# Kernel tuning notes

Hardware: AMD Instinct MI355X
Metric: run time of the kernel (lower is better)

## Reference

```python
import jax, jax.numpy as jnp
import numpy as np

DIM = 512
HEADS = 8
HEAD = DIM // HEADS
T = 243          # temporal length, fixed by get_temporal_mask(243, ...)
N_JOINTS = 17    # skeleton joints
BATCH = 4        # number of clips; leading dim of x is BATCH*T
WINDOWS = (9, 27, 81, 243)  # temporal_MoE_type


def _temporal_masks():
    # Block-diagonal window masks: 0 inside each window block, -100000 outside,
    # exactly matching get_temporal_mask + torch.where(matrix == 0, -100000, 0).
    idx = np.arange(T)
    masks = np.stack([
        np.where((idx[:, None] // w) == (idx[None, :] // w), 0.0, -100000.0)
        for w in WINDOWS
    ]).astype(np.float32)  # (E, T, T)
    return jnp.asarray(masks)


def setup_inputs() -> dict:
    key = jax.random.key(0)
    k0, k1, k2, k3 = jax.random.split(key, 4)
    scaled = lambda k, shape, fan: jax.random.normal(k, shape, jnp.float32) * (fan ** -0.5)
    return {
        "x": jax.random.normal(k0, (BATCH * T, N_JOINTS, DIM), jnp.float32),
        "qkv_w": scaled(k1, (DIM, 3 * DIM), DIM),          # qkv (no bias, qkv_bias=False)
        "proj_w": scaled(k2, (DIM, DIM), DIM),             # output projection
        "proj_b": jnp.zeros((DIM,), jnp.float32),
        "te_w": scaled(k3, (DIM, len(WINDOWS)), DIM),      # temporal_expert_linear
        "te_b": jnp.zeros((len(WINDOWS),), jnp.float32),
        "seqlen": T,
    }


def reference(x, qkv_w, proj_w, proj_b, te_w, te_b, seqlen):
    BT, n, C = x.shape              # (b*T, N, C)
    b = BT // seqlen
    scale = HEAD ** -0.5
    # qkv projection -> q,k,v each (b, H, N, T, head_dim)
    qkv = (x @ qkv_w).reshape(b, seqlen, n, 3, HEADS, HEAD)
    qkv = jnp.transpose(qkv, (3, 0, 4, 2, 1, 5))  # (3, b, H, N, T, c)
    q, k, v = qkv[0], qkv[1], qkv[2]
    # temporal attention logits, shared across experts: (b, H, N, T, T)
    attn = jnp.einsum('bhntc,bhnsc->bhnts', q, k) * scale
    masks = _temporal_masks()                       # (E, T, T)
    attn = attn[None] + masks[:, None, None, None]  # (E, b, H, N, T, T)
    attn = jax.nn.softmax(attn, axis=-1)            # attn_drop is identity (p=0 / eval)
    eo = jnp.einsum('ebhnts,bhnsc->ebhntc', attn, v)
    E = masks.shape[0]
    # (E,b,H,N,T,c) -> (E,b,T,N,H,c) -> (E, b*T, N, C), matching permute(0,3,2,1,4)
    eo = jnp.transpose(eo, (0, 1, 4, 3, 2, 5)).reshape(E, BT, n, C)
    # expert gating: softmax(temporal_expert_linear(x)) over experts, per token
    w = jax.nn.softmax(x @ te_w + te_b, axis=-1)    # (BT, N, E)
    out = jnp.einsum('ebnc,bne->bnc', eo, w)        # fused expert recombination
    out = out @ proj_w + proj_b                     # proj (proj_drop identity)
    return out
```

## Files before the change

### kernel.cpp

```cpp
#include <hip/hip_runtime.h>
#include <hip/hip_bf16.h>
#include <cstdint>

#define TT 243
#define NJ 17
#define NB 4
#define NH 8
#define HD 64
#define CDIM 512
#define NROWS (NB*TT*NJ)
#define NBHN (NB*NH*NJ)

typedef unsigned short u16;
typedef __attribute__((ext_vector_type(8))) short short8;
typedef __attribute__((ext_vector_type(4))) float f32x4;

#define MFMA16(a, b, c) __builtin_amdgcn_mfma_f32_16x16x32_bf16((a), (b), (c), 0, 0, 0)

__device__ __forceinline__ void gl_lds16(const void* g, void* l) {
  __builtin_amdgcn_global_load_lds(
      (const __attribute__((address_space(1))) void*)g,
      (__attribute__((address_space(3))) void*)l, 16, 0, 0);
}

__device__ __forceinline__ u16 f2bf(float f) {
  union { float f; unsigned u; } v; v.f = f;
  unsigned r = v.u + 0x7FFFu + ((v.u >> 16) & 1u);
  return (u16)(r >> 16);
}

__device__ __forceinline__ float wave_reduce_sum(float v) {
#pragma unroll
  for (int off = 32; off > 0; off >>= 1) v += __shfl_xor(v, off, 64);
  return v;
}

__global__ __launch_bounds__(256) void convgates(
    const float* __restrict__ x, const float* __restrict__ te_w,
    const float* __restrict__ te_b, u16* __restrict__ xb,
    float* __restrict__ gates) {
  int w = threadIdx.x >> 6, l = threadIdx.x & 63;
  int row = blockIdx.x * 4 + w;
  if (row >= NROWS) return;
  const float* xr = x + (size_t)row * CDIM;
  u16* xo = xb + (size_t)row * CDIM;
  float a0 = 0.f, a1 = 0.f, a2 = 0.f, a3 = 0.f;
#pragma unroll
  for (int p = 0; p < 2; ++p) {
    int c = (p * 64 + l) * 4;
    float4 v = *(const float4*)(xr + c);
    ushort4 o;
    o.x = f2bf(v.x); o.y = f2bf(v.y); o.z = f2bf(v.z); o.w = f2bf(v.w);
    *(ushort4*)(xo + c) = o;
    float xv[4] = {v.x, v.y, v.z, v.w};
#pragma unroll
    for (int q = 0; q < 4; ++q) {
      float4 wv = *(const float4*)(te_w + (size_t)(c + q) * 4);
      a0 += xv[q] * wv.x; a1 += xv[q] * wv.y;
      a2 += xv[q] * wv.z; a3 += xv[q] * wv.w;
    }
  }
  a0 = wave_reduce_sum(a0);
  a1 = wave_reduce_sum(a1);
  a2 = wave_reduce_sum(a2);
  a3 = wave_reduce_sum(a3);
  a0 += te_b[0]; a1 += te_b[1]; a2 += te_b[2]; a3 += te_b[3];
  float mx = fmaxf(fmaxf(a0, a1), fmaxf(a2, a3));
  float e0 = __expf(a0 - mx), e1 = __expf(a1 - mx);
  float e2 = __expf(a2 - mx), e3 = __expf(a3 - mx);
  float inv = 1.f / (e0 + e1 + e2 + e3);
  if (l == 0) {
    *(float4*)(gates + (size_t)row * 4) =
        make_float4(e0 * inv, e1 * inv, e2 * inv, e3 * inv);
  }
}

__global__ __launch_bounds__(256) void trans_w(const float* __restrict__ in,
                                               u16* __restrict__ out, int K, int N) {
  __shared__ float tile[32][33];
  int n0 = blockIdx.x * 32, k0 = blockIdx.y * 32;
  int tx = threadIdx.x & 31, ty = threadIdx.x >> 5;
#pragma unroll
  for (int p = 0; p < 4; ++p)
    tile[ty + p * 8][tx] = in[(size_t)(k0 + ty + p * 8) * N + n0 + tx];
  __syncthreads();
#pragma unroll
  for (int p = 0; p < 4; ++p)
    out[(size_t)(n0 + ty + p * 8) * K + k0 + tx] = f2bf(tile[tx][ty + p * 8]);
}

__global__ __launch_bounds__(256) void qkv_gemm(
    const u16* __restrict__ xb, const u16* __restrict__ wt,
    u16* __restrict__ qh, u16* __restrict__ kh, u16* __restrict__ vb) {
  __shared__ u16 S[16640];
  u16* Al = S;
  u16* Bl = S + 8192;
  int tid = threadIdx.x;
  int w = tid >> 6, l = tid & 63;
  int c16 = tid & 15, g4 = (tid >> 4) & 3;
  int r0 = blockIdx.x * 128, n0 = blockIdx.y * 128;
  int wm = w & 1, wn = w >> 1;

  size_t arow[2]; int ac8[2], brow[2];
#pragma unroll
  for (int it = 0; it < 2; ++it) {
    int F = it * 256 + w * 64 + l;
    int row = F >> 2;
    ac8[it] = F & 3;
    brow[it] = n0 + row;
    int m = r0 + row; if (m >= NROWS) m = NROWS - 1;
    int bj = m / 243, t = m - bj * 243;
    int b = bj / 17, j = bj - b * 17;
    arow[it] = ((size_t)(b * 243 + t) * 17 + j) * 512;
  }

  f32x4 acc[4][4] = {};
  for (int k0 = 0; k0 < CDIM; k0 += 32) {
    __syncthreads();
#pragma unroll
    for (int it = 0; it < 2; ++it) {
      gl_lds16(xb + arow[it] + k0 + ac8[it] * 8,
               Al + (size_t)(it * 256 + w * 64) * 8);
      gl_lds16(wt + (size_t)brow[it] * 512 + k0 + ac8[it] * 8,
               Bl + (size_t)(it * 256 + w * 64) * 8);
    }
    __syncthreads();
    short8 af[4], bf[4];
#pragma unroll
    for (int i = 0; i < 4; ++i)
      af[i] = *(const short8*)(Al + ((wm * 64 + i * 16 + c16) * 32 + g4 * 8));
#pragma unroll
    for (int j = 0; j < 4; ++j)
      bf[j] = *(const short8*)(Bl + ((wn * 64 + j * 16 + c16) * 32 + g4 * 8));
#pragma unroll
    for (int i = 0; i < 4; ++i)
#pragma unroll
      for (int j = 0; j < 4; ++j)
        acc[i][j] = MFMA16(af[i], bf[j], acc[i][j]);
  }

  if (n0 < 1024) {
#pragma unroll
    for (int i = 0; i < 4; ++i)
#pragma unroll
      for (int r = 0; r < 4; ++r) {
        int m = r0 + wm * 64 + i * 16 + g4 * 4 + r;
        if (m >= NROWS) continue;
        int bj = m / 243, t = m - bj * 243;
        int b = bj / 17, j = bj - b * 17;
#pragma unroll
        for (int jt = 0; jt < 4; ++jt) {
          int col = n0 + wn * 64 + jt * 16 + c16;
          int sel = col >> 9, h = (col >> 6) & 7, c = col & 63;
          u16* dst = sel ? kh : qh;
          dst[((size_t)((b * 8 + h) * 17 + j) * 243 + t) * 64 + c] =
              f2bf(acc[i][jt][r]);
        }
      }
  } else {
    __syncthreads();
#pragma unroll
    for (int i = 0; i < 4; ++i)
#pragma unroll
      for (int jt = 0; jt < 4; ++jt)
#pragma unroll
        for (int r = 0; r < 4; ++r) {
          int row = wm * 64 + i * 16 + g4 * 4 + r;
          int colI = wn * 64 + jt * 16 + c16;
          S[colI * 130 + row] = f2bf(acc[i][jt][r]);
        }
    __syncthreads();
    int hb = (n0 - 1024) >> 6;
    int m0 = r0 + 2 * l;
    int m1 = m0 + 1;
    bool v0 = m0 < NROWS, v1 = m1 < NROWS;
    int bj0 = m0 / 243, t0 = m0 - bj0 * 243;
    int b0 = bj0 / 17, j0 = bj0 - b0 * 17;
    int bj1 = m1 / 243, t1 = m1 - bj1 * 243;
    int b1 = bj1 / 17, j1 = bj1 - b1 * 17;
    size_t base0 = ((size_t)(b0 * 136 + j0) * 64) * 256 + t0;
    size_t base1 = ((size_t)(b1 * 136 + j1) * 64) * 256 + t1;
#pragma unroll 8
    for (int cc = 0; cc < 32; ++cc) {
      int colI = w * 32 + cc;
      int h = hb + (colI >> 6), c = colI & 63;
      ushort2 u = *(const ushort2*)&S[colI * 130 + 2 * l];
      size_t hoff = ((size_t)h * 17 * 64) * 256 + (size_t)c * 256;
      if (v0) vb[base0 + hoff] = u.x;
      if (v1) vb[base1 + hoff] = u.y;
    }
  }
}

__global__ __launch_bounds__(256, 4) void attn_kernel(
    const u16* __restrict__ qh, const u16* __restrict__ kh,
    const u16* __restrict__ vb, const float* __restrict__ gates,
    u16* __restrict__ preb) {
  __shared__ u16 L[16384];
  int bhn = blockIdx.x;
  int q0 = blockIdx.y * 64;
  int b = bhn / (NH * NJ);
  int hj = bhn - b * (NH * NJ);
  int h = hj / NJ, j = hj - h * NJ;
  int tid = threadIdx.x;
  int w = tid >> 6;
  int c16 = tid & 15, g4 = (tid >> 4) & 3;
  const u16* Kp = kh + (size_t)bhn * (TT * HD);
  const u16* Qp = qh + (size_t)bhn * (TT * HD);
  const u16* Vp = vb + (size_t)bhn * (HD * 256);
  u16* Rw = L + w * 4096;

#pragma unroll
  for (int it = 0; it < 8; ++it) {
    int F = it * 256 + tid;
    int s = F >> 3;
    int c8 = (F & 7) ^ (s & 7);
    int sg = s < TT ? s : TT - 1;
    gl_lds16(Kp + (size_t)sg * 64 + c8 * 8, L + (size_t)(it * 256 + (tid & ~63)) * 8);
  }
  __syncthreads();

  int qrow = q0 + w * 16 + c16;
  int qg = qrow < TT ? qrow : TT - 1;
  short8 aq[2];
#pragma unroll
  for (int hh = 0; hh < 2; ++hh)
    aq[hh] = *(const short8*)(Qp + (size_t)qg * 64 + hh * 32 + g4 * 8);

  f32x4 acc[16];
#pragma unroll
  for (int st = 0; st < 16; ++st) acc[st] = (f32x4)(0.f);
#pragma unroll
  for (int st = 0; st < 16; ++st) {
    int s = st * 16 + c16;
#pragma unroll
    for (int hh = 0; hh < 2; ++hh) {
      short8 bk = *(const short8*)(L + s * 64 + ((hh * 4 + g4) ^ (s & 7)) * 8);
      acc[st] = MFMA16(aq[hh], bk, acc[st]);
    }
  }
  __syncthreads();

  int tr[4], t9[4], t27[4], t81[4];
#pragma unroll
  for (int r = 0; r < 4; ++r) {
    tr[r] = q0 + w * 16 + g4 * 4 + r;
    t9[r] = tr[r] / 9; t27[r] = t9[r] / 3; t81[r] = t27[r] / 3;
  }
#pragma unroll
  for (int st = 0; st < 16; ++st) {
    int s = st * 16 + c16;
#pragma unroll
    for (int r = 0; r < 4; ++r) {
      float v = acc[st][r] * 0.125f;
      acc[st][r] = (s < TT) ? v : -1e30f;
    }
  }
  float M[4];
#pragma unroll
  for (int r = 0; r < 4; ++r) {
    float m = -1e30f;
#pragma unroll
    for (int st = 0; st < 16; ++st) m = fmaxf(m, acc[st][r]);
    m = fmaxf(m, __shfl_xor(m, 1, 64));
    m = fmaxf(m, __shfl_xor(m, 2, 64));
    m = fmaxf(m, __shfl_xor(m, 4, 64));
    m = fmaxf(m, __shfl_xor(m, 8, 64));
    M[r] = m;
  }
#pragma unroll
  for (int st = 0; st < 16; ++st)
#pragma unroll
    for (int r = 0; r < 4; ++r) acc[st][r] = __expf(acc[st][r] - M[r]);
  int s9[16], s27[16], s81[16];
#pragma unroll
  for (int st = 0; st < 16; ++st) {
    int s = st * 16 + c16;
    s9[st] = s / 9; s27[st] = s9[st] / 3; s81[st] = s27[st] / 3;
  }
  float l9[4], l27[4], l81[4], l243[4];
#pragma unroll
  for (int r = 0; r < 4; ++r) { l9[r] = 0.f; l27[r] = 0.f; l81[r] = 0.f; l243[r] = 0.f; }
#pragma unroll
  for (int st = 0; st < 16; ++st)
#pragma unroll
    for (int r = 0; r < 4; ++r) {
      float e = acc[st][r];
      l243[r] += e;
      l9[r]  += (s9[st]  == t9[r])  ? e : 0.f;
      l27[r] += (s27[st] == t27[r]) ? e : 0.f;
      l81[r] += (s81[st] == t81[r]) ? e : 0.f;
    }
#pragma unroll
  for (int r = 0; r < 4; ++r) {
#pragma unroll
    for (int d = 1; d <= 8; d <<= 1) {
      l9[r]   += __shfl_xor(l9[r], d, 64);
      l27[r]  += __shfl_xor(l27[r], d, 64);
      l81[r]  += __shfl_xor(l81[r], d, 64);
      l243[r] += __shfl_xor(l243[r], d, 64);
    }
  }
  float c0[4], c1[4], c2[4], c3[4];
#pragma unroll
  for (int r = 0; r < 4; ++r) {
    int tg = tr[r] < TT ? tr[r] : TT - 1;
    float4 g = *(const float4*)(gates + ((size_t)(b * TT + tg) * NJ + j) * 4);
    c0[r] = g.x / l9[r]; c1[r] = g.y / l27[r];
    c2[r] = g.z / l81[r]; c3[r] = g.w / l243[r];
  }
#pragma unroll
  for (int st = 0; st < 16; ++st) {
    int s = st * 16 + c16;
#pragma unroll
    for (int r = 0; r < 4; ++r) {
      float cw = c3[r];
      cw += (s81[st] == t81[r]) ? c2[r] : 0.f;
      cw += (s27[st] == t27[r]) ? c1[r] : 0.f;
      cw += (s9[st]  == t9[r])  ? c0[r] : 0.f;
      float rv = acc[st][r] * cw;
      if (tr[r] >= TT || s >= TT) rv = 0.f;
      int q = g4 * 4 + r;
      int s8 = s >> 3;
      int slot = (s8 & 24) | ((s8 & 7) ^ (q & 7));
      Rw[q * 256 + slot * 8 + (s & 7)] = f2bf(rv);
    }
  }

  short8 ar[8];
#pragma unroll
  for (int h2 = 0; h2 < 8; ++h2) {
    int cc = h2 * 4 + g4;
    int slot = (cc & 24) | ((cc & 7) ^ (c16 & 7));
    ar[h2] = *(const short8*)(Rw + c16 * 256 + slot * 8);
  }
#pragma unroll
  for (int jt = 0; jt < 4; ++jt) {
    int c = jt * 16 + c16;
    f32x4 o = (f32x4)(0.f);
#pragma unroll
    for (int h2 = 0; h2 < 8; ++h2) {
      short8 bv = *(const short8*)(Vp + (size_t)c * 256 + h2 * 32 + g4 * 8);
      o = MFMA16(ar[h2], bv, o);
    }
#pragma unroll
    for (int r = 0; r < 4; ++r) {
      int t = tr[r];
      if (t < TT)
        preb[((size_t)(b * TT + t) * NJ + j) * 512 + h * 64 + c] = f2bf(o[r]);
    }
  }
}

__global__ __launch_bounds__(256) void proj_gemm(
    const u16* __restrict__ preb, const u16* __restrict__ pwt,
    const float* __restrict__ bias, float* __restrict__ out) {
  __shared__ u16 Al[128 * 32];
  __shared__ u16 Bl[128 * 32];
  int tid = threadIdx.x;
  int w = tid >> 6, l = tid & 63;
  int c16 = tid & 15, g4 = (tid >> 4) & 3;
  int r0 = blockIdx.x * 128, n0 = blockIdx.y * 128;
  int wm = w & 1, wn = w >> 1;
  f32x4 acc[4][4] = {};
  for (int k0 = 0; k0 < CDIM; k0 += 32) {
    __syncthreads();
#pragma unroll
    for (int it = 0; it < 2; ++it) {
      int F = it * 256 + w * 64 + l;
      int row = F >> 2, c8 = F & 3;
      int gr = r0 + row; gr = gr < NROWS ? gr : NROWS - 1;
      gl_lds16(preb + (size_t)gr * 512 + k0 + c8 * 8,
               Al + (size_t)(it * 256 + w * 64) * 8);
      gl_lds16(pwt + (size_t)(n0 + row) * 512 + k0 + c8 * 8,
               Bl + (size_t)(it * 256 + w * 64) * 8);
    }
    __syncthreads();
    short8 af[4], bf[4];
#pragma unroll
    for (int i = 0; i < 4; ++i)
      af[i] = *(const short8*)(Al + ((wm * 64 + i * 16 + c16) * 32 + g4 * 8));
#pragma unroll
    for (int j = 0; j < 4; ++j)
      bf[j] = *(const short8*)(Bl + ((wn * 64 + j * 16 + c16) * 32 + g4 * 8));
#pragma unroll
    for (int i = 0; i < 4; ++i)
#pragma unroll
      for (int j = 0; j < 4; ++j)
        acc[i][j] = MFMA16(af[i], bf[j], acc[i][j]);
  }
#pragma unroll
  for (int i = 0; i < 4; ++i)
#pragma unroll
    for (int r = 0; r < 4; ++r) {
      int row = r0 + wm * 64 + i * 16 + g4 * 4 + r;
      if (row >= NROWS) continue;
#pragma unroll
      for (int jt = 0; jt < 4; ++jt) {
        int col = n0 + wn * 64 + jt * 16 + c16;
        out[(size_t)row * 512 + col] = acc[i][jt][r] + bias[col];
      }
    }
}

extern "C" void kernel_launch(void* const* d_in, const int* in_sizes, int n_in,
                              void* d_out, int out_size, void* d_ws, size_t ws_size,
                              hipStream_t stream) {
  (void)in_sizes; (void)n_in; (void)out_size; (void)ws_size;
  const float* x      = (const float*)d_in[0];
  const float* qkv_w  = (const float*)d_in[1];
  const float* proj_w = (const float*)d_in[2];
  const float* proj_b = (const float*)d_in[3];
  const float* te_w   = (const float*)d_in[4];
  const float* te_b   = (const float*)d_in[5];

  char* p = (char*)d_ws;
  auto alloc = [&](size_t bytes) {
    void* r = (void*)p;
    p += (bytes + 255) & ~(size_t)255;
    return r;
  };
  u16*   xb    = (u16*)alloc((size_t)NROWS * 512 * 2);
  u16*   wt    = (u16*)alloc((size_t)1536 * 512 * 2);
  u16*   pwt   = (u16*)alloc((size_t)512 * 512 * 2);
  float* gates = (float*)alloc((size_t)NROWS * 4 * 4);
  u16*   qhb   = (u16*)alloc((size_t)NBHN * 243 * 64 * 2);
  u16*   khb   = (u16*)alloc((size_t)NBHN * 243 * 64 * 2);
  u16*   vb    = (u16*)alloc((size_t)NBHN * 64 * 256 * 2);
  u16*   preb  = (u16*)alloc((size_t)NROWS * 512 * 2);
  float* out   = (float*)d_out;

  hipLaunchKernelGGL(convgates, dim3((NROWS + 3) / 4), dim3(256), 0, stream,
                     x, te_w, te_b, xb, gates);
  hipLaunchKernelGGL(trans_w, dim3(48, 16), dim3(256), 0, stream,
                     qkv_w, wt, 512, 1536);
  hipLaunchKernelGGL(trans_w, dim3(16, 16), dim3(256), 0, stream,
                     proj_w, pwt, 512, 512);
  hipLaunchKernelGGL(qkv_gemm, dim3((NROWS + 127) / 128, 12), dim3(256), 0, stream,
                     xb, wt, qhb, khb, vb);
  hipLaunchKernelGGL(attn_kernel, dim3(NBHN, 4), dim3(256), 0, stream,
                     qhb, khb, vb, gates, preb);
  hipLaunchKernelGGL(proj_gemm, dim3((NROWS + 127) / 128, 4), dim3(256), 0, stream,
                     preb, pwt, proj_b, out);
}
```

Before: 241.5 us.

## Transpose QK^T MFMA, fold softmax scale into Q, simplify window gating

Folds the 1/sqrt(d)*log2(e) scale into Q at the QKV GEMM epilogue so the attention kernel can use exp2f directly. It also swaps the MFMA operands so each lane owns a single query row, which cuts the max and sum reductions to two shuffles. Window membership tests and cumulative gate coefficients replace per-element integer divisions, and P is written to LDS as packed 8-byte stores. The GEMM grids are reordered so that blocks sharing a row tile run adjacently, with the aim of better A-tile cache reuse.

```diff
diff --git a/kernel.cpp b/kernel.cpp
--- a/kernel.cpp
+++ b/kernel.cpp
@@ -16,6 +16,7 @@
 typedef __attribute__((ext_vector_type(4))) float f32x4;
 
 #define MFMA16(a, b, c) __builtin_amdgcn_mfma_f32_16x16x32_bf16((a), (b), (c), 0, 0, 0)
+#define QSCALE 0.18033688011112042f
 
 __device__ __forceinline__ void gl_lds16(const void* g, void* l) {
   __builtin_amdgcn_global_load_lds(
@@ -98,7 +99,7 @@
   int tid = threadIdx.x;
   int w = tid >> 6, l = tid & 63;
   int c16 = tid & 15, g4 = (tid >> 4) & 3;
-  int r0 = blockIdx.x * 128, n0 = blockIdx.y * 128;
+  int r0 = blockIdx.y * 128, n0 = blockIdx.x * 128;
   int wm = w & 1, wn = w >> 1;
 
   size_t arow[2]; int ac8[2], brow[2];
@@ -153,8 +154,9 @@
           int col = n0 + wn * 64 + jt * 16 + c16;
           int sel = col >> 9, h = (col >> 6) & 7, c = col & 63;
           u16* dst = sel ? kh : qh;
-          dst[((size_t)((b * 8 + h) * 17 + j) * 243 + t) * 64 + c] =
-              f2bf(acc[i][jt][r]);
+          float val = acc[i][jt][r];
+          if (!sel) val *= QSCALE;
+          dst[((size_t)((b * 8 + h) * 17 + j) * 243 + t) * 64 + c] = f2bf(val);
         }
       }
   } else {
@@ -220,111 +222,92 @@
   }
   __syncthreads();
 
-  int qrow = q0 + w * 16 + c16;
-  int qg = qrow < TT ? qrow : TT - 1;
-  short8 aq[2];
+  int tt = q0 + w * 16 + c16;
+  bool tvalid = tt < TT;
+  int tg = tvalid ? tt : TT - 1;
+
+  short8 bq[2];
 #pragma unroll
   for (int hh = 0; hh < 2; ++hh)
-    aq[hh] = *(const short8*)(Qp + (size_t)qg * 64 + hh * 32 + g4 * 8);
+    bq[hh] = *(const short8*)(Qp + (size_t)tg * 64 + hh * 32 + g4 * 8);
 
   f32x4 acc[16];
 #pragma unroll
   for (int st = 0; st < 16; ++st) acc[st] = (f32x4)(0.f);
 #pragma unroll
   for (int st = 0; st < 16; ++st) {
-    int s = st * 16 + c16;
+    int sf = st * 16 + c16;
 #pragma unroll
     for (int hh = 0; hh < 2; ++hh) {
-      short8 bk = *(const short8*)(L + s * 64 + ((hh * 4 + g4) ^ (s & 7)) * 8);
-      acc[st] = MFMA16(aq[hh], bk, acc[st]);
+      short8 ak = *(const short8*)(L + sf * 64 + ((hh * 4 + g4) ^ (sf & 7)) * 8);
+      acc[st] = MFMA16(ak, bq[hh], acc[st]);
     }
   }
   __syncthreads();
 
-  int tr[4], t9[4], t27[4], t81[4];
-#pragma unroll
-  for (int r = 0; r < 4; ++r) {
-    tr[r] = q0 + w * 16 + g4 * 4 + r;
-    t9[r] = tr[r] / 9; t27[r] = t9[r] / 3; t81[r] = t27[r] / 3;
-  }
+  float M = -1e30f;
+#pragma unroll
+  for (int st = 0; st < 16; ++st)
+#pragma unroll
+    for (int r = 0; r < 4; ++r) {
+      int s = st * 16 + g4 * 4 + r;
+      float v = acc[st][r];
+      v = (s < TT) ? v : -1e30f;
+      acc[st][r] = v;
+      M = fmaxf(M, v);
+    }
+  M = fmaxf(M, __shfl_xor(M, 16, 64));
+  M = fmaxf(M, __shfl_xor(M, 32, 64));
+
+#pragma unroll
+  for (int st = 0; st < 16; ++st)
+#pragma unroll
+    for (int r = 0; r < 4; ++r) acc[st][r] = exp2f(acc[st][r] - M);
+
+  int t9b = (tg / 9) * 9;
+  int t27b = (tg / 27) * 27;
+  int t81b = (tg / 81) * 81;
+  float l9 = 0.f, l27 = 0.f, l81 = 0.f, l243 = 0.f;
+#pragma unroll
+  for (int st = 0; st < 16; ++st)
+#pragma unroll
+    for (int r = 0; r < 4; ++r) {
+      int s = st * 16 + g4 * 4 + r;
+      float e = acc[st][r];
+      l243 += e;
+      l81 += ((unsigned)(s - t81b) < 81u) ? e : 0.f;
+      l27 += ((unsigned)(s - t27b) < 27u) ? e : 0.f;
+      l9  += ((unsigned)(s - t9b)  <  9u) ? e : 0.f;
+    }
+  l9   += __shfl_xor(l9, 16, 64);   l9   += __shfl_xor(l9, 32, 64);
+  l27  += __shfl_xor(l27, 16, 64);  l27  += __shfl_xor(l27, 32, 64);
+  l81  += __shfl_xor(l81, 16, 64);  l81  += __shfl_xor(l81, 32, 64);
+  l243 += __shfl_xor(l243, 16, 64); l243 += __shfl_xor(l243, 32, 64);
+
+  float4 gv = *(const float4*)(gates + ((size_t)(b * TT + tg) * NJ + j) * 4);
+  float gam3 = gv.w / l243;
+  float gam2 = gam3 + gv.z / l81;
+  float gam1 = gam2 + gv.y / l27;
+  float gam0 = gam1 + gv.x / l9;
+
 #pragma unroll
   for (int st = 0; st < 16; ++st) {
-    int s = st * 16 + c16;
+    float rv[4];
 #pragma unroll
     for (int r = 0; r < 4; ++r) {
-      float v = acc[st][r] * 0.125f;
-      acc[st][r] = (s < TT) ? v : -1e30f;
-    }
-  }
-  float M[4];
-#pragma unroll
-  for (int r = 0; r < 4; ++r) {
-    float m = -1e30f;
-#pragma unroll
-    for (int st = 0; st < 16; ++st) m = fmaxf(m, acc[st][r]);
-    m = fmaxf(m, __shfl_xor(m, 1, 64));
-    m = fmaxf(m, __shfl_xor(m, 2, 64));
-    m = fmaxf(m, __shfl_xor(m, 4, 64));
-    m = fmaxf(m, __shfl_xor(m, 8, 64));
-    M[r] = m;
-  }
-#pragma unroll
-  for (int st = 0; st < 16; ++st)
-#pragma unroll
-    for (int r = 0; r < 4; ++r) acc[st][r] = __expf(acc[st][r] - M[r]);
-  int s9[16], s27[16], s81[16];
-#pragma unroll
-  for (int st = 0; st < 16; ++st) {
-    int s = st * 16 + c16;
-    s9[st] = s / 9; s27[st] = s9[st] / 3; s81[st] = s27[st] / 3;
-  }
-  float l9[4], l27[4], l81[4], l243[4];
-#pragma unroll
-  for (int r = 0; r < 4; ++r) { l9[r] = 0.f; l27[r] = 0.f; l81[r] = 0.f; l243[r] = 0.f; }
-#pragma unroll
-  for (int st = 0; st < 16; ++st)
-#pragma unroll
-    for (int r = 0; r < 4; ++r) {
+      int s = st * 16 + g4 * 4 + r;
       float e = acc[st][r];
-      l243[r] += e;
-      l9[r]  += (s9[st]  == t9[r])  ? e : 0.f;
-      l27[r] += (s27[st] == t27[r]) ? e : 0.f;
-      l81[r] += (s81[st] == t81[r]) ? e : 0.f;
-    }
-#pragma unroll
-  for (int r = 0; r < 4; ++r) {
-#pragma unroll
-    for (int d = 1; d <= 8; d <<= 1) {
-      l9[r]   += __shfl_xor(l9[r], d, 64);
-      l27[r]  += __shfl_xor(l27[r], d, 64);
-      l81[r]  += __shfl_xor(l81[r], d, 64);
-      l243[r] += __shfl_xor(l243[r], d, 64);
-    }
-  }
-  float c0[4], c1[4], c2[4], c3[4];
-#pragma unroll
-  for (int r = 0; r < 4; ++r) {
-    int tg = tr[r] < TT ? tr[r] : TT - 1;
-    float4 g = *(const float4*)(gates + ((size_t)(b * TT + tg) * NJ + j) * 4);
-    c0[r] = g.x / l9[r]; c1[r] = g.y / l27[r];
-    c2[r] = g.z / l81[r]; c3[r] = g.w / l243[r];
-  }
-#pragma unroll
-  for (int st = 0; st < 16; ++st) {
-    int s = st * 16 + c16;
-#pragma unroll
-    for (int r = 0; r < 4; ++r) {
-      float cw = c3[r];
-      cw += (s81[st] == t81[r]) ? c2[r] : 0.f;
-      cw += (s27[st] == t27[r]) ? c1[r] : 0.f;
-      cw += (s9[st]  == t9[r])  ? c0[r] : 0.f;
-      float rv = acc[st][r] * cw;
-      if (tr[r] >= TT || s >= TT) rv = 0.f;
-      int q = g4 * 4 + r;
-      int s8 = s >> 3;
-      int slot = (s8 & 24) | ((s8 & 7) ^ (q & 7));
-      Rw[q * 256 + slot * 8 + (s & 7)] = f2bf(rv);
-    }
+      float cw = ((unsigned)(s - t9b) < 9u) ? gam0
+               : ((unsigned)(s - t27b) < 27u) ? gam1
+               : ((unsigned)(s - t81b) < 81u) ? gam2 : gam3;
+      rv[r] = tvalid ? e * cw : 0.f;
+    }
+    uint2 pk;
+    pk.x = (unsigned)f2bf(rv[0]) | ((unsigned)f2bf(rv[1]) << 16);
+    pk.y = (unsigned)f2bf(rv[2]) | ((unsigned)f2bf(rv[3]) << 16);
+    int c8 = st * 2 + (g4 >> 1);
+    int slot = (c8 & 24) | ((c8 & 7) ^ (c16 & 7));
+    *(uint2*)(Rw + c16 * 256 + slot * 8 + (g4 & 1) * 4) = pk;
   }
 
   short8 ar[8];
@@ -345,7 +328,7 @@
     }
 #pragma unroll
     for (int r = 0; r < 4; ++r) {
-      int t = tr[r];
+      int t = q0 + w * 16 + g4 * 4 + r;
       if (t < TT)
         preb[((size_t)(b * TT + t) * NJ + j) * 512 + h * 64 + c] = f2bf(o[r]);
     }
@@ -360,7 +343,7 @@
   int tid = threadIdx.x;
   int w = tid >> 6, l = tid & 63;
   int c16 = tid & 15, g4 = (tid >> 4) & 3;
-  int r0 = blockIdx.x * 128, n0 = blockIdx.y * 128;
+  int r0 = blockIdx.y * 128, n0 = blockIdx.x * 128;
   int wm = w & 1, wn = w >> 1;
   f32x4 acc[4][4] = {};
   for (int k0 = 0; k0 < CDIM; k0 += 32) {
@@ -436,10 +419,10 @@
                      qkv_w, wt, 512, 1536);
   hipLaunchKernelGGL(trans_w, dim3(16, 16), dim3(256), 0, stream,
                      proj_w, pwt, 512, 512);
-  hipLaunchKernelGGL(qkv_gemm, dim3((NROWS + 127) / 128, 12), dim3(256), 0, stream,
+  hipLaunchKernelGGL(qkv_gemm, dim3(12, (NROWS + 127) / 128), dim3(256), 0, stream,
                      xb, wt, qhb, khb, vb);
   hipLaunchKernelGGL(attn_kernel, dim3(NBHN, 4), dim3(256), 0, stream,
                      qhb, khb, vb, gates, preb);
-  hipLaunchKernelGGL(proj_gemm, dim3((NROWS + 127) / 128, 4), dim3(256), 0, stream,
+  hipLaunchKernelGGL(proj_gemm, dim3(4, (NROWS + 127) / 128), dim3(256), 0, stream,
                      preb, pwt, proj_b, out);
 }
```

New measurement: 233.7 us. -3.2%, faster.
